# Kernel optimization log

Hardware: AMD Instinct MI355X
Metric: run time of the kernel (lower is better)

## Reference

```python
import jax, jax.numpy as jnp
import numpy as np


def setup_inputs() -> dict:
    key = jax.random.key(0)
    ks = jax.random.split(key, 10)
    B, C, W, H = 4, 128, 64, 64
    c_half = C // 2          # 64
    d_qk = c_half // 8       # 8 (ratio=8)
    c_out = c_half           # 64
    inp = {
        "x":   jax.random.normal(ks[0], (B, C, W, H), jnp.float32),
        # att2.query_conv (used for both q2 and k2)
        "wq2": jax.random.normal(ks[1], (d_qk, c_half), jnp.float32) * 0.05,
        "bq2": jax.random.normal(ks[2], (d_qk,), jnp.float32) * 0.05,
        # att3.query_conv (used for both q3 and k3)
        "wq3": jax.random.normal(ks[3], (d_qk, c_half), jnp.float32) * 0.05,
        "bq3": jax.random.normal(ks[4], (d_qk,), jnp.float32) * 0.05,
        # att3.value_conv
        "wv3": jax.random.normal(ks[5], (c_out, c_half), jnp.float32) * 0.05,
        "bv3": jax.random.normal(ks[6], (c_out,), jnp.float32) * 0.05,
        # gammas are zero-init in torch; use small random so output is non-trivial
        "gamma2": jax.random.normal(ks[7], (1,), jnp.float32) * 0.1,
        "gamma3": jax.random.normal(ks[8], (1,), jnp.float32) * 0.1,
    }
    return inp


def reference(x, wq2, bq2, wq3, bq3, wv3, bv3, gamma2, gamma3):
    B, C, W, H = x.shape
    c_half = C // 2
    N = W * H
    x3 = x[:, :c_half].reshape(B, c_half, N)   # [B, C/2, N]
    x2 = x[:, c_half:].reshape(B, c_half, N)

    def conv1x1(w, b, inp):  # [O,Ci] x [B,Ci,N] -> [B,O,N]
        return jnp.einsum('oc,bcn->bon', w, inp) + b[None, :, None]

    p2 = conv1x1(wq2, bq2, x2)   # [B, d, N]  (q2 and k2 share this projection)
    p3 = conv1x1(wq3, bq3, x3)   # [B, d, N]  (q3 and k3 share this projection)
    v3 = conv1x1(wv3, bv3, x3)   # [B, Cout, N]

    # energy: q3^T @ k  -> [B, N, N]; softmax over last dim (no scaling)
    att32 = jax.nn.softmax(jnp.einsum('bdm,bdn->bmn', p3, p2), axis=-1)
    att33 = jax.nn.softmax(jnp.einsum('bdm,bdn->bmn', p3, p3), axis=-1)

    # out = v3 @ att^T : out[b,c,m] = sum_n v3[b,c,n] * att[b,m,n]
    out32 = jnp.einsum('bcn,bmn->bcm', v3, att32)
    out33 = jnp.einsum('bcn,bmn->bcm', v3, att33)

    out = gamma2 * out32 + gamma3 * out33 + x3   # add=True
    return out.reshape(B, c_half, W, H)
```

## Files before the change

kernel.cpp:

```cpp
#include <hip/hip_runtime.h>

#define NN 4096
#define BB 4

typedef short v8s __attribute__((ext_vector_type(8)));
typedef float v4f __attribute__((ext_vector_type(4)));

__device__ __forceinline__ float bf2f(unsigned short u) {
  union { unsigned int i; float f; } v;
  v.i = ((unsigned int)u) << 16;
  return v.f;
}
__device__ __forceinline__ unsigned short f2bf(float f) {
  union { float f; unsigned int i; } v;
  v.f = f;
  unsigned int r = v.i + 0x7FFFu + ((v.i >> 16) & 1u);
  return (unsigned short)(r >> 16);
}
__device__ __forceinline__ unsigned int pkbf(float hi, float lo) {
  union { float f; unsigned int u; } a, b;
  a.f = hi; b.f = lo;
  return __builtin_amdgcn_perm(a.u, b.u, 0x07060302u);
}

__device__ __forceinline__ float ldv(const float* p, size_t i) { return p[i]; }
__device__ __forceinline__ float ldv(const unsigned short* p, size_t i) { return bf2f(p[i]); }

template <int NPL>
__device__ __forceinline__ bool sniff_f32(const unsigned short* xu) {
  const int lane = threadIdx.x & 63;
  int cnt = 0;
  #pragma unroll
  for (int j = 0; j < NPL; j++) {
    unsigned short u = xu[lane * NPL + j];
    cnt += (((u >> 7) & 0xFF) >= 137) ? 1 : 0;
  }
  #pragma unroll
  for (int s = 1; s < 64; s <<= 1) cnt += __shfl_xor(cnt, s);
  return cnt > NPL;
}

template <typename T>
__device__ __forceinline__ void proj_body(
    const T* __restrict__ x,
    const T* __restrict__ wq2, const T* __restrict__ bq2,
    const T* __restrict__ wq3, const T* __restrict__ bq3,
    const T* __restrict__ wv3, const T* __restrict__ bv3,
    unsigned short* __restrict__ p2bf, unsigned short* __restrict__ p3bf,
    unsigned short* __restrict__ v3bf)
{
  const int tid  = threadIdx.x;
  const int col  = tid & 63;
  const int part = tid >> 6;
  const int bid  = blockIdx.x;
  const int b    = bid >> 6;
  const int n    = ((bid & 63) << 6) | col;
  const size_t xcol = (size_t)b * 128 * NN + n;

  float xc[64];

  #pragma unroll
  for (int c = 0; c < 64; c++) xc[c] = ldv(x, xcol + (size_t)(64 + c) * NN);
  {
    float a01[2];
    #pragma unroll
    for (int dd = 0; dd < 2; dd++) {
      const int d = part * 2 + dd;
      float acc = ldv(bq2, d);
      #pragma unroll
      for (int c = 0; c < 64; c++) acc = fmaf(ldv(wq2, d * 64 + c), xc[c], acc);
      a01[dd] = acc;
    }
    *(unsigned int*)(p2bf + ((size_t)b * NN + n) * 8 + part * 2) = pkbf(a01[1], a01[0]);
  }

  #pragma unroll
  for (int c = 0; c < 64; c++) xc[c] = ldv(x, xcol + (size_t)c * NN);
  {
    float a01[2];
    #pragma unroll
    for (int dd = 0; dd < 2; dd++) {
      const int d = part * 2 + dd;
      float acc = ldv(bq3, d);
      #pragma unroll
      for (int c = 0; c < 64; c++) acc = fmaf(ldv(wq3, d * 64 + c), xc[c], acc);
      a01[dd] = acc;
    }
    *(unsigned int*)(p3bf + ((size_t)b * NN + n) * 8 + part * 2) = pkbf(a01[1], a01[0]);
  }
  for (int i = 0; i < 16; i++) {
    const int co = part * 16 + i;
    float acc = ldv(bv3, co);
    #pragma unroll
    for (int c = 0; c < 64; c++) acc = fmaf(ldv(wv3, co * 64 + c), xc[c], acc);
    v3bf[((size_t)b * 64 + co) * NN + n] = f2bf(acc);
  }
}

__global__ __launch_bounds__(256) void proj_kernel(
    const void* __restrict__ x,
    const void* __restrict__ wq2, const void* __restrict__ bq2,
    const void* __restrict__ wq3, const void* __restrict__ bq3,
    const void* __restrict__ wv3, const void* __restrict__ bv3,
    unsigned short* __restrict__ p2bf, unsigned short* __restrict__ p3bf,
    unsigned short* __restrict__ v3bf)
{
  const bool f32 = sniff_f32<16>((const unsigned short*)x);
  if (f32)
    proj_body<float>((const float*)x, (const float*)wq2, (const float*)bq2,
                     (const float*)wq3, (const float*)bq3,
                     (const float*)wv3, (const float*)bv3, p2bf, p3bf, v3bf);
  else
    proj_body<unsigned short>((const unsigned short*)x, (const unsigned short*)wq2,
                              (const unsigned short*)bq2, (const unsigned short*)wq3,
                              (const unsigned short*)bq3, (const unsigned short*)wv3,
                              (const unsigned short*)bv3, p2bf, p3bf, v3bf);
}

__global__ __launch_bounds__(256, 4) void attn_kernel(
    const unsigned short* __restrict__ p2bf, const unsigned short* __restrict__ p3bf,
    const unsigned short* __restrict__ v3bf,
    unsigned short* __restrict__ wso, float* __restrict__ wsl,
    int log2S, int nChunks)
{
  __shared__ unsigned short vtile[64 * 72];
  __shared__ unsigned short p2t[64 * 8];
  __shared__ unsigned short p3t[64 * 8];
  __shared__ unsigned short etile[4][2][16 * 72];

  const int tid  = threadIdx.x;
  const int lane = tid & 63;
  const int w    = tid >> 6;
  const int q    = lane >> 4;
  const int l15  = lane & 15;
  const int bid  = blockIdx.x;
  const int S    = 1 << log2S;
  const int seg  = bid & (S - 1);
  const int t    = bid >> log2S;
  const int mt   = t & 63;
  const int b    = t >> 6;
  const int m    = (mt << 6) + w * 16 + l15;

  v8s b3m = {0, 0, 0, 0, 0, 0, 0, 0};
  if (q == 0) b3m = *(const v8s*)(p3bf + ((size_t)b * NN + m) * 8);

  v4f acc32[4], acc33[4];
  #pragma unroll
  for (int ct = 0; ct < 4; ct++)
    #pragma unroll
    for (int r = 0; r < 4; r++) { acc32[ct][r] = 0.f; acc33[ct][r] = 0.f; }
  float ls2 = 0.f, ls3 = 0.f;

  const int n_base = seg * (nChunks * 64);
  unsigned short* et2 = &etile[w][0][0];
  unsigned short* et3 = &etile[w][1][0];

  const int vrow = tid >> 3, vseg = tid & 7;
  uint4 vreg0, vreg1, preg;

  {
    const int n0 = n_base;
    vreg0 = *(const uint4*)(v3bf + ((size_t)b * 64 + vrow) * NN + n0 + vseg * 8);
    vreg1 = *(const uint4*)(v3bf + ((size_t)b * 64 + (vrow + 32)) * NN + n0 + vseg * 8);
    if (tid < 64)       preg = *(const uint4*)(p2bf + ((size_t)b * NN + n0 + tid) * 8);
    else if (tid < 128) preg = *(const uint4*)(p3bf + ((size_t)b * NN + n0 + (tid - 64)) * 8);
  }

  for (int ci = 0; ci < nChunks; ci++) {
    __syncthreads();
    *(uint4*)(vtile + vrow * 72 + vseg * 8)        = vreg0;
    *(uint4*)(vtile + (vrow + 32) * 72 + vseg * 8) = vreg1;
    if (tid < 64)       *(uint4*)(p2t + tid * 8)        = preg;
    else if (tid < 128) *(uint4*)(p3t + (tid - 64) * 8) = preg;
    __syncthreads();

    if (ci + 1 < nChunks) {
      const int n1 = n_base + (ci + 1) * 64;
      vreg0 = *(const uint4*)(v3bf + ((size_t)b * 64 + vrow) * NN + n1 + vseg * 8);
      vreg1 = *(const uint4*)(v3bf + ((size_t)b * 64 + (vrow + 32)) * NN + n1 + vseg * 8);
      if (tid < 64)       preg = *(const uint4*)(p2bf + ((size_t)b * NN + n1 + tid) * 8);
      else if (tid < 128) preg = *(const uint4*)(p3bf + ((size_t)b * NN + n1 + (tid - 64)) * 8);
    }

    #pragma unroll
    for (int s = 0; s < 4; s++) {
      v8s A2 = {0, 0, 0, 0, 0, 0, 0, 0};
      v8s A3 = {0, 0, 0, 0, 0, 0, 0, 0};
      if (q == 0) {
        A2 = *(const v8s*)(p2t + (s * 16 + l15) * 8);
        A3 = *(const v8s*)(p3t + (s * 16 + l15) * 8);
      }
      v4f z = {0.f, 0.f, 0.f, 0.f};
      v4f e2 = __builtin_amdgcn_mfma_f32_16x16x32_bf16(A2, b3m, z, 0, 0, 0);
      v4f e3 = __builtin_amdgcn_mfma_f32_16x16x32_bf16(A3, b3m, z, 0, 0, 0);
      float t2[4], t3[4];
      #pragma unroll
      for (int r = 0; r < 4; r++) {
        t2[r] = __expf(e2[r]);
        t3[r] = __expf(e3[r]);
        ls2 += t2[r];
        ls3 += t3[r];
      }
      uint2 w2, w3;
      w2.x = pkbf(t2[1], t2[0]); w2.y = pkbf(t2[3], t2[2]);
      w3.x = pkbf(t3[1], t3[0]); w3.y = pkbf(t3[3], t3[2]);
      *(uint2*)(et2 + l15 * 72 + s * 16 + q * 4) = w2;
      *(uint2*)(et3 + l15 * 72 + s * 16 + q * 4) = w3;
    }

    #pragma unroll
    for (int kh = 0; kh < 2; kh++) {
      v8s at2 = *(const v8s*)(et2 + l15 * 72 + kh * 32 + q * 8);
      v8s at3 = *(const v8s*)(et3 + l15 * 72 + kh * 32 + q * 8);
      #pragma unroll
      for (int ct = 0; ct < 4; ct++) {
        v8s va = *(const v8s*)(vtile + (ct * 16 + l15) * 72 + kh * 32 + q * 8);
        acc32[ct] = __builtin_amdgcn_mfma_f32_16x16x32_bf16(va, at2, acc32[ct], 0, 0, 0);
        acc33[ct] = __builtin_amdgcn_mfma_f32_16x16x32_bf16(va, at3, acc33[ct], 0, 0, 0);
      }
    }
  }

  ls2 += __shfl_xor(ls2, 16); ls2 += __shfl_xor(ls2, 32);
  ls3 += __shfl_xor(ls3, 16); ls3 += __shfl_xor(ls3, 32);
  if (q == 0) {
    wsl[((size_t)bid * 2 + 0) * 64 + w * 16 + l15] = ls2;
    wsl[((size_t)bid * 2 + 1) * 64 + w * 16 + l15] = ls3;
  }
  const int m6 = w * 16 + l15;
  #pragma unroll
  for (int ct = 0; ct < 4; ct++) {
    uint2 o2, o3;
    o2.x = pkbf(acc32[ct][1], acc32[ct][0]); o2.y = pkbf(acc32[ct][3], acc32[ct][2]);
    o3.x = pkbf(acc33[ct][1], acc33[ct][0]); o3.y = pkbf(acc33[ct][3], acc33[ct][2]);
    *(uint2*)(wso + (((size_t)bid * 2 + 0) * 64 + m6) * 64 + ct * 16 + q * 4) = o2;
    *(uint2*)(wso + (((size_t)bid * 2 + 1) * 64 + m6) * 64 + ct * 16 + q * 4) = o3;
  }
}

__global__ __launch_bounds__(256) void reduce_kernel(
    const unsigned short* __restrict__ wso, const float* __restrict__ wsl,
    const void* __restrict__ x, const void* __restrict__ g2p,
    const void* __restrict__ g3p, void* __restrict__ out, int S)
{
  __shared__ float t32[64 * 65];
  __shared__ float t33[64 * 65];
  __shared__ float iL2s[64], iL3s[64];

  const bool f32 = sniff_f32<4>((const unsigned short*)x);
  const int tid = threadIdx.x;
  const int mt  = blockIdx.x & 63;
  const int b   = blockIdx.x >> 6;
  const size_t blk0 = (size_t)((b << 6) + mt) * S;

  #pragma unroll
  for (int k = 0; k < 4; k++) {
    const int idx = tid + k * 256;
    const int m6 = idx >> 4;
    const int cg = idx & 15;
    float o2[4] = {0.f, 0.f, 0.f, 0.f}, o3[4] = {0.f, 0.f, 0.f, 0.f};
    for (int sg = 0; sg < S; sg++) {
      const uint2 u2 = *(const uint2*)(wso + ((blk0 + sg) * 2 + 0) * 4096 + m6 * 64 + cg * 4);
      const uint2 u3 = *(const uint2*)(wso + ((blk0 + sg) * 2 + 1) * 4096 + m6 * 64 + cg * 4);
      union { unsigned int u; float f; } c0, c1, c2, c3;
      c0.u = u2.x << 16; c1.u = u2.x & 0xFFFF0000u; c2.u = u2.y << 16; c3.u = u2.y & 0xFFFF0000u;
      o2[0] += c0.f; o2[1] += c1.f; o2[2] += c2.f; o2[3] += c3.f;
      c0.u = u3.x << 16; c1.u = u3.x & 0xFFFF0000u; c2.u = u3.y << 16; c3.u = u3.y & 0xFFFF0000u;
      o3[0] += c0.f; o3[1] += c1.f; o3[2] += c2.f; o3[3] += c3.f;
    }
    #pragma unroll
    for (int j = 0; j < 4; j++) {
      t32[m6 * 65 + cg * 4 + j] = o2[j];
      t33[m6 * 65 + cg * 4 + j] = o3[j];
    }
  }
  if (tid < 64) {
    float L2 = 0.f, L3 = 0.f;
    for (int sg = 0; sg < S; sg++) {
      L2 += wsl[((blk0 + sg) * 2 + 0) * 64 + tid];
      L3 += wsl[((blk0 + sg) * 2 + 1) * 64 + tid];
    }
    const float g2 = f32 ? ((const float*)g2p)[0] : bf2f(((const unsigned short*)g2p)[0]);
    const float g3 = f32 ? ((const float*)g3p)[0] : bf2f(((const unsigned short*)g3p)[0]);
    iL2s[tid] = g2 / L2;
    iL3s[tid] = g3 / L3;
  }
  __syncthreads();

  const int m6 = tid & 63;
  const int ch = tid >> 6;
  #pragma unroll
  for (int k = 0; k < 16; k++) {
    const int c = k * 4 + ch;
    const size_t xi = ((size_t)b * 128 + c) * NN + (mt << 6) + m6;
    const float xv = f32 ? ((const float*)x)[xi] : bf2f(((const unsigned short*)x)[xi]);
    const float val = fmaf(iL2s[m6], t32[m6 * 65 + c], fmaf(iL3s[m6], t33[m6 * 65 + c], xv));
    const size_t oi = ((size_t)b * 64 + c) * NN + (mt << 6) + m6;
    if (f32) ((float*)out)[oi] = val;
    else     ((unsigned short*)out)[oi] = f2bf(val);
  }
}

extern "C" void kernel_launch(void* const* d_in, const int* in_sizes, int n_in,
                              void* d_out, int out_size, void* d_ws, size_t ws_size,
                              hipStream_t stream) {
  const void* x   = d_in[0];
  const void* wq2 = d_in[1];
  const void* bq2 = d_in[2];
  const void* wq3 = d_in[3];
  const void* bq3 = d_in[4];
  const void* wv3 = d_in[5];
  const void* bv3 = d_in[6];
  const void* g2  = d_in[7];
  const void* g3  = d_in[8];

  unsigned short* p2bf = (unsigned short*)d_ws;
  unsigned short* p3bf = p2bf + (size_t)BB * NN * 8;
  unsigned short* v3bf = p3bf + (size_t)BB * NN * 8;
  const size_t base = 2 * (size_t)BB * NN * 8 * 2 + (size_t)BB * 64 * NN * 2;

  const size_t per_blk = 512 + 16384;
  int S = 1, log2S = 0;
  if      (ws_size >= base + (size_t)256 * 8 * per_blk) { S = 8; log2S = 3; }
  else if (ws_size >= base + (size_t)256 * 4 * per_blk) { S = 4; log2S = 2; }
  else if (ws_size >= base + (size_t)256 * 2 * per_blk) { S = 2; log2S = 1; }

  float* wsl = (float*)((char*)d_ws + base);
  unsigned short* wso = (unsigned short*)((char*)wsl + (size_t)256 * S * 512);
  const int nChunks = 64 / S;

  proj_kernel<<<dim3(BB * 64), dim3(256), 0, stream>>>(
      x, wq2, bq2, wq3, bq3, wv3, bv3, p2bf, p3bf, v3bf);
  attn_kernel<<<dim3(BB * 64 * S), dim3(256), 0, stream>>>(
      p2bf, p3bf, v3bf, wso, wsl, log2S, nChunks);
  reduce_kernel<<<dim3(BB * 64), dim3(256), 0, stream>>>(
      wso, wsl, x, g2, g3, d_out, S);
}
```

Before: 150.6 us.

## Move projections and softmax row sums onto MFMA, fold log2e into weights

The 1x1 projection kernel is rewritten so the q/k and value projections run as bf16 MFMA tiles instead of per-thread scalar FMA loops. The q/k weights and biases are prescaled by log2(e) so the attention kernel can use exp2f instead of __expf. Softmax denominators are now accumulated with an MFMA against a ones vector over the bf16 probability tiles, replacing per-lane scalar sums and shuffles. Inputs and weights are rounded to bf16 before projection, which adds precision loss relative to fp32 FMA, and the row sums now come from bf16-rounded exponentials.

```diff
diff --git a/kernel.cpp b/kernel.cpp
--- a/kernel.cpp
+++ b/kernel.cpp
@@ -39,6 +39,8 @@
   for (int s = 1; s < 64; s <<= 1) cnt += __shfl_xor(cnt, s);
   return cnt > NPL;
 }
+
+#define QK_SCALE 1.2011224087864498f
 
 template <typename T>
 __device__ __forceinline__ void proj_body(
@@ -50,51 +52,77 @@
     unsigned short* __restrict__ v3bf)
 {
   const int tid  = threadIdx.x;
-  const int col  = tid & 63;
-  const int part = tid >> 6;
+  const int lane = tid & 63;
+  const int w    = tid >> 6;
+  const int q    = lane >> 4;
+  const int l15  = lane & 15;
   const int bid  = blockIdx.x;
   const int b    = bid >> 6;
-  const int n    = ((bid & 63) << 6) | col;
-  const size_t xcol = (size_t)b * 128 * NN + n;
-
-  float xc[64];
-
-  #pragma unroll
-  for (int c = 0; c < 64; c++) xc[c] = ldv(x, xcol + (size_t)(64 + c) * NN);
-  {
-    float a01[2];
-    #pragma unroll
-    for (int dd = 0; dd < 2; dd++) {
-      const int d = part * 2 + dd;
-      float acc = ldv(bq2, d);
+  const int nt   = bid & 63;
+  const int n    = (nt << 6) + w * 16 + l15;
+
+  v8s aq2[2], aq3[2], av[4][2];
+  #pragma unroll
+  for (int ks = 0; ks < 2; ks++) {
+    const int c0 = ks * 32 + q * 8;
+    #pragma unroll
+    for (int j = 0; j < 8; j++) {
+      const int wrow = (l15 < 8) ? l15 : 0;
+      const float w2 = ldv(wq2, wrow * 64 + c0 + j);
+      const float w3 = ldv(wq3, wrow * 64 + c0 + j);
+      aq2[ks][j] = (l15 < 8) ? (short)f2bf(QK_SCALE * w2) : (short)0;
+      aq3[ks][j] = (l15 < 8) ? (short)f2bf(QK_SCALE * w3) : (short)0;
+    }
+    #pragma unroll
+    for (int t = 0; t < 4; t++) {
       #pragma unroll
-      for (int c = 0; c < 64; c++) acc = fmaf(ldv(wq2, d * 64 + c), xc[c], acc);
-      a01[dd] = acc;
-    }
-    *(unsigned int*)(p2bf + ((size_t)b * NN + n) * 8 + part * 2) = pkbf(a01[1], a01[0]);
-  }
-
-  #pragma unroll
-  for (int c = 0; c < 64; c++) xc[c] = ldv(x, xcol + (size_t)c * NN);
-  {
-    float a01[2];
-    #pragma unroll
-    for (int dd = 0; dd < 2; dd++) {
-      const int d = part * 2 + dd;
-      float acc = ldv(bq3, d);
-      #pragma unroll
-      for (int c = 0; c < 64; c++) acc = fmaf(ldv(wq3, d * 64 + c), xc[c], acc);
-      a01[dd] = acc;
-    }
-    *(unsigned int*)(p3bf + ((size_t)b * NN + n) * 8 + part * 2) = pkbf(a01[1], a01[0]);
-  }
-  for (int i = 0; i < 16; i++) {
-    const int co = part * 16 + i;
-    float acc = ldv(bv3, co);
-    #pragma unroll
-    for (int c = 0; c < 64; c++) acc = fmaf(ldv(wv3, co * 64 + c), xc[c], acc);
-    v3bf[((size_t)b * 64 + co) * NN + n] = f2bf(acc);
-  }
+      for (int j = 0; j < 8; j++)
+        av[t][ks][j] = (short)f2bf(ldv(wv3, (t * 16 + l15) * 64 + c0 + j));
+    }
+  }
+
+  v4f ap2, ap3, avc[4];
+  #pragma unroll
+  for (int r = 0; r < 4; r++) {
+    const int ob = (q < 2) ? q * 4 + r : 0;
+    const float b2 = ldv(bq2, ob), b3 = ldv(bq3, ob);
+    ap2[r] = (q < 2) ? QK_SCALE * b2 : 0.f;
+    ap3[r] = (q < 2) ? QK_SCALE * b3 : 0.f;
+  }
+  #pragma unroll
+  for (int t = 0; t < 4; t++)
+    #pragma unroll
+    for (int r = 0; r < 4; r++) avc[t][r] = ldv(bv3, t * 16 + q * 4 + r);
+
+  const size_t xb = (size_t)b * 128 * NN + n;
+  #pragma unroll
+  for (int ks = 0; ks < 2; ks++) {
+    const int c0 = ks * 32 + q * 8;
+    v8s bx2, bx3;
+    #pragma unroll
+    for (int j = 0; j < 8; j++) {
+      bx2[j] = (short)f2bf(ldv(x, xb + (size_t)(64 + c0 + j) * NN));
+      bx3[j] = (short)f2bf(ldv(x, xb + (size_t)(c0 + j) * NN));
+    }
+    ap2 = __builtin_amdgcn_mfma_f32_16x16x32_bf16(aq2[ks], bx2, ap2, 0, 0, 0);
+    ap3 = __builtin_amdgcn_mfma_f32_16x16x32_bf16(aq3[ks], bx3, ap3, 0, 0, 0);
+    #pragma unroll
+    for (int t = 0; t < 4; t++)
+      avc[t] = __builtin_amdgcn_mfma_f32_16x16x32_bf16(av[t][ks], bx3, avc[t], 0, 0, 0);
+  }
+
+  if (q < 2) {
+    uint2 u2, u3;
+    u2.x = pkbf(ap2[1], ap2[0]); u2.y = pkbf(ap2[3], ap2[2]);
+    u3.x = pkbf(ap3[1], ap3[0]); u3.y = pkbf(ap3[3], ap3[2]);
+    *(uint2*)(p2bf + ((size_t)b * NN + n) * 8 + q * 4) = u2;
+    *(uint2*)(p3bf + ((size_t)b * NN + n) * 8 + q * 4) = u3;
+  }
+  #pragma unroll
+  for (int t = 0; t < 4; t++)
+    #pragma unroll
+    for (int r = 0; r < 4; r++)
+      v3bf[((size_t)b * 64 + t * 16 + q * 4 + r) * NN + n] = f2bf(avc[t][r]);
 }
 
 __global__ __launch_bounds__(256) void proj_kernel(
@@ -144,12 +172,15 @@
   v8s b3m = {0, 0, 0, 0, 0, 0, 0, 0};
   if (q == 0) b3m = *(const v8s*)(p3bf + ((size_t)b * NN + m) * 8);
 
-  v4f acc32[4], acc33[4];
+  const v8s ones = {16256, 16256, 16256, 16256, 16256, 16256, 16256, 16256};
+
+  v4f acc32[4], acc33[4], lac2, lac3;
   #pragma unroll
   for (int ct = 0; ct < 4; ct++)
     #pragma unroll
     for (int r = 0; r < 4; r++) { acc32[ct][r] = 0.f; acc33[ct][r] = 0.f; }
-  float ls2 = 0.f, ls3 = 0.f;
+  #pragma unroll
+  for (int r = 0; r < 4; r++) { lac2[r] = 0.f; lac3[r] = 0.f; }
 
   const int n_base = seg * (nChunks * 64);
   unsigned short* et2 = &etile[w][0][0];
@@ -196,10 +227,8 @@
       float t2[4], t3[4];
       #pragma unroll
       for (int r = 0; r < 4; r++) {
-        t2[r] = __expf(e2[r]);
-        t3[r] = __expf(e3[r]);
-        ls2 += t2[r];
-        ls3 += t3[r];
+        t2[r] = exp2f(e2[r]);
+        t3[r] = exp2f(e3[r]);
       }
       uint2 w2, w3;
       w2.x = pkbf(t2[1], t2[0]); w2.y = pkbf(t2[3], t2[2]);
@@ -212,6 +241,8 @@
     for (int kh = 0; kh < 2; kh++) {
       v8s at2 = *(const v8s*)(et2 + l15 * 72 + kh * 32 + q * 8);
       v8s at3 = *(const v8s*)(et3 + l15 * 72 + kh * 32 + q * 8);
+      lac2 = __builtin_amdgcn_mfma_f32_16x16x32_bf16(ones, at2, lac2, 0, 0, 0);
+      lac3 = __builtin_amdgcn_mfma_f32_16x16x32_bf16(ones, at3, lac3, 0, 0, 0);
       #pragma unroll
       for (int ct = 0; ct < 4; ct++) {
         v8s va = *(const v8s*)(vtile + (ct * 16 + l15) * 72 + kh * 32 + q * 8);
@@ -221,11 +252,9 @@
     }
   }
 
-  ls2 += __shfl_xor(ls2, 16); ls2 += __shfl_xor(ls2, 32);
-  ls3 += __shfl_xor(ls3, 16); ls3 += __shfl_xor(ls3, 32);
   if (q == 0) {
-    wsl[((size_t)bid * 2 + 0) * 64 + w * 16 + l15] = ls2;
-    wsl[((size_t)bid * 2 + 1) * 64 + w * 16 + l15] = ls3;
+    wsl[((size_t)bid * 2 + 0) * 64 + w * 16 + l15] = lac2[0];
+    wsl[((size_t)bid * 2 + 1) * 64 + w * 16 + l15] = lac3[0];
   }
   const int m6 = w * 16 + l15;
   #pragma unroll
```

Result: no change. 148.8 us (-1.2%).
